# Kernel optimization log

Measured on AMD Instinct MI355X. Metric: run time of the kernel, lower is better.

The kernel has to match this reference:

```python
import jax, jax.numpy as jnp
import numpy as np

B, S, F, E, K = 4, 1024, 1024, 8, 2
H = 4 * F  # expert hidden dim, hard-coded as features*4 in the module


def setup_inputs() -> dict:
    key = jax.random.key(0)
    ks = jax.random.split(key, 7)
    def xavier(k, shape):
        fan_in, fan_out = shape[-2], shape[-1]
        scale = jnp.sqrt(6.0 / (fan_in + fan_out))
        return jax.random.uniform(k, shape, jnp.float32, -scale, scale)
    return {
        "x": jax.random.normal(ks[0], (B, S, F), jnp.float32),
        "Wg": xavier(ks[1], (F, E)),
        "bg": jnp.zeros((E,), jnp.float32),
        "W1": xavier(ks[2], (E, F, H)),
        "b1": jnp.zeros((E, H), jnp.float32),
        "W2": xavier(ks[3], (E, H, F)),
        "b2": jnp.zeros((E, F), jnp.float32),
    }


def reference(x, Wg, bg, W1, b1, W2, b2):
    # Gating: softmax over experts, keep top-k, renormalize.
    gate_probs = jax.nn.softmax(x @ Wg + bg, axis=-1)              # (b,s,E)
    k = K
    _, top_idx = jax.lax.top_k(gate_probs, k)                       # (b,s,k)
    expert_mask = jax.nn.one_hot(top_idx, gate_probs.shape[-1],
                                 dtype=gate_probs.dtype).sum(-2)    # (b,s,E)
    selected = gate_probs * expert_mask
    selected = selected / (selected.sum(-1, keepdims=True) + 1e-8)
    # Dense all-expert 2-layer MLP (gelu, tanh approximation as in flax nn.gelu).
    h = jax.nn.gelu(jnp.einsum('bsf,efh->bseh', x, W1) + b1)        # (b,s,E,H)
    expert_out = jnp.einsum('bseh,ehf->bsef', h, W2) + b2[None, None]  # (b,s,E,F)
    # Weighted combine over experts with renormalized top-k gates.
    return jnp.einsum('bsef,bse->bsf', expert_out, selected)
```

## Files before the change

kernel.cpp:

```cpp
#include <hip/hip_runtime.h>
#include <hip/hip_bf16.h>

constexpr int Ff = 1024;
constexpr int Ee = 8;
constexpr int Hh = 4096;
constexpr int T  = 4096;
constexpr int MB = 80;

typedef short     bf16x8 __attribute__((ext_vector_type(8)));
typedef float     f32x4  __attribute__((ext_vector_type(4)));
typedef unsigned short u16x8 __attribute__((ext_vector_type(8)));

__device__ __forceinline__ float gelu_fast(float v) {
  const float c2 = 2.0f * 0.7978845608028654f;
  float z2 = c2 * (v + 0.044715f * v * v * v);
  return v / (1.0f + __expf(-z2));
}

__device__ __forceinline__ unsigned short bf16bits(float f) {
  __hip_bfloat16 h = __float2bfloat16(f);
  return *reinterpret_cast<unsigned short*>(&h);
}

__device__ __forceinline__ void gl_lds16(const void* g, void* l) {
  __builtin_amdgcn_global_load_lds(
      (const __attribute__((address_space(1))) unsigned int*)g,
      (__attribute__((address_space(3))) unsigned int*)l, 16, 0, 0);
}

__global__ __launch_bounds__(256) void gating_kernel(
    const float* __restrict__ x, const float* __restrict__ Wg,
    const float* __restrict__ bg, int* __restrict__ cnt,
    int* __restrict__ list, float* __restrict__ wlist,
    int* __restrict__ done, int* __restrict__ offs) {
  const int wave = threadIdx.x >> 6;
  const int lane = threadIdx.x & 63;
  const int t = blockIdx.x * 4 + wave;
  float acc[Ee] = {0.f,0.f,0.f,0.f,0.f,0.f,0.f,0.f};
  const float* xrow = x + (size_t)t * Ff;
  for (int f0 = 0; f0 < Ff; f0 += 64) {
    float xv = xrow[f0 + lane];
    const float* wrow = Wg + (size_t)(f0 + lane) * Ee;
    float4 w0 = *reinterpret_cast<const float4*>(wrow);
    float4 w1 = *reinterpret_cast<const float4*>(wrow + 4);
    acc[0] += xv * w0.x; acc[1] += xv * w0.y;
    acc[2] += xv * w0.z; acc[3] += xv * w0.w;
    acc[4] += xv * w1.x; acc[5] += xv * w1.y;
    acc[6] += xv * w1.z; acc[7] += xv * w1.w;
  }
#pragma unroll
  for (int e = 0; e < Ee; ++e) {
#pragma unroll
    for (int off = 32; off; off >>= 1) acc[e] += __shfl_xor(acc[e], off);
  }
  if (lane == 0) {
    float l[Ee], m = -1e30f;
#pragma unroll
    for (int e = 0; e < Ee; ++e) { l[e] = acc[e] + bg[e]; m = fmaxf(m, l[e]); }
    float p[Ee], Z = 0.f;
#pragma unroll
    for (int e = 0; e < Ee; ++e) { p[e] = expf(l[e] - m); Z += p[e]; }
#pragma unroll
    for (int e = 0; e < Ee; ++e) p[e] /= Z;
    int i1 = 0; float p1 = p[0];
#pragma unroll
    for (int e = 1; e < Ee; ++e) if (p[e] > p1) { p1 = p[e]; i1 = e; }
    int i2 = -1; float p2 = -1e30f;
#pragma unroll
    for (int e = 0; e < Ee; ++e) if (e != i1 && p[e] > p2) { p2 = p[e]; i2 = e; }
    float denom = p1 + p2 + 1e-8f;
    int pos = atomicAdd(&cnt[i1], 1);
    list[i1 * T + pos] = t; wlist[i1 * T + pos] = p1 / denom;
    pos = atomicAdd(&cnt[i2], 1);
    list[i2 * T + pos] = t; wlist[i2 * T + pos] = p2 / denom;
  }
  __syncthreads();
  if (threadIdx.x == 0) {
    __threadfence();
    if (atomicAdd(done, 1) == gridDim.x - 1) {
      int s = 0;
#pragma unroll
      for (int e = 0; e < Ee; ++e) {
        offs[e] = s;
        s += (atomicAdd(&cnt[e], 0) + 127) & ~127;
      }
      offs[Ee] = s;
    }
  }
}

__global__ __launch_bounds__(256) void pack_w_kernel(
    const float* __restrict__ src1, unsigned short* __restrict__ dst1,
    int sN1, size_t s_estride1, size_t d_estride1, int KT1v, int NB1,
    const float* __restrict__ src2, unsigned short* __restrict__ dst2,
    int sN2, size_t s_estride2, size_t d_estride2, int KT2v, int NB2,
    int n1) {
  int idx = blockIdx.x;
  const float* src; unsigned short* dst;
  int sN, KT, nb, kt, e;
  size_t s_estride, d_estride;
  if (idx < n1) {
    src = src1; dst = dst1; sN = sN1; KT = KT1v;
    s_estride = s_estride1; d_estride = d_estride1;
    e = idx / (NB1 * KT1v); int r = idx % (NB1 * KT1v);
    nb = r / KT1v; kt = r % KT1v;
  } else {
    idx -= n1;
    src = src2; dst = dst2; sN = sN2; KT = KT2v;
    s_estride = s_estride2; d_estride = d_estride2;
    e = idx / (NB2 * KT2v); int r = idx % (NB2 * KT2v);
    nb = r / KT2v; kt = r % KT2v;
  }
  __shared__ float Ts[128][33];
  const int t = threadIdx.x;
  const float* sb = src + (size_t)e * s_estride + (size_t)(kt * 32) * sN + nb * 128;
  {
    const int row = t >> 5;
    const int cc  = (t & 31) * 4;
#pragma unroll
    for (int i = 0; i < 4; ++i) {
      float4 v = *reinterpret_cast<const float4*>(sb + (size_t)(row + 8 * i) * sN + cc);
      Ts[cc + 0][row + 8 * i] = v.x;
      Ts[cc + 1][row + 8 * i] = v.y;
      Ts[cc + 2][row + 8 * i] = v.z;
      Ts[cc + 3][row + 8 * i] = v.w;
    }
  }
  __syncthreads();
  unsigned short* db = dst + (size_t)e * d_estride + ((size_t)nb * KT + kt) * 4096;
#pragma unroll
  for (int j = 0; j < 2; ++j) {
    const int i2 = t + 256 * j;
    const int col = i2 & 127, kb = i2 >> 7;
    u16x8 o;
#pragma unroll
    for (int q = 0; q < 8; ++q) o[q] = bf16bits(Ts[col][kb * 8 + q]);
    *reinterpret_cast<u16x8*>(db + kb * 1024 + col * 8) = o;
  }
}

__global__ __launch_bounds__(256) void pack_x_kernel(
    const float* __restrict__ x, const int* __restrict__ cnt,
    const int* __restrict__ offs, const int* __restrict__ list,
    unsigned short* __restrict__ xg) {
  const int kt = blockIdx.x;
  const int mb = blockIdx.y;
  const int t = threadIdx.x;
  const int m0g = mb * 128;
  int e = 0;
#pragma unroll
  for (int i = 1; i < Ee; ++i) e += (m0g >= offs[i]) ? 1 : 0;
  const int ce = cnt[e];
  const int row = t >> 1, half = t & 1;
  const int mloc = m0g - offs[e] + row;
  const bool valid = (mloc >= 0) && (mloc < ce);
  const int token = valid ? list[e * T + mloc] : 0;
  const float* sp = x + (size_t)token * Ff + kt * 32 + half * 16;
  u16x8 o0, o1;
#pragma unroll
  for (int i = 0; i < 2; ++i) {
    float4 v = valid ? *reinterpret_cast<const float4*>(sp + i * 4)
                     : make_float4(0.f, 0.f, 0.f, 0.f);
    o0[i * 4 + 0] = bf16bits(v.x); o0[i * 4 + 1] = bf16bits(v.y);
    o0[i * 4 + 2] = bf16bits(v.z); o0[i * 4 + 3] = bf16bits(v.w);
  }
#pragma unroll
  for (int i = 2; i < 4; ++i) {
    float4 v = valid ? *reinterpret_cast<const float4*>(sp + i * 4)
                     : make_float4(0.f, 0.f, 0.f, 0.f);
    o1[(i - 2) * 4 + 0] = bf16bits(v.x); o1[(i - 2) * 4 + 1] = bf16bits(v.y);
    o1[(i - 2) * 4 + 2] = bf16bits(v.z); o1[(i - 2) * 4 + 3] = bf16bits(v.w);
  }
  unsigned short* db = xg + ((size_t)mb * (Ff / 32) + kt) * 4096 + row * 8;
  *reinterpret_cast<u16x8*>(db + (half * 2 + 0) * 1024) = o0;
  *reinterpret_cast<u16x8*>(db + (half * 2 + 1) * 1024) = o1;
}

__global__ __launch_bounds__(256, 3) void gemm1_mfma(
    const unsigned short* __restrict__ xg, const unsigned short* __restrict__ W1P,
    const float* __restrict__ b1, const int* __restrict__ cnt,
    const int* __restrict__ offs, unsigned short* __restrict__ hp, int Hc, int c) {
  const int nxg = Hc >> 7;
  const int nwg = nxg * MB;
  const int raw = blockIdx.x;
  int bid = (raw & 7) * (nwg >> 3) + (raw >> 3);
  const int bw = (nxg >= 4) ? 4 : nxg;
  const int band = bid / (MB * bw);
  const int r2 = bid % (MB * bw);
  const int by = r2 / bw;
  const int bx = band * bw + (r2 % bw);

  const int m0g = by * 128;
  int e = 0;
#pragma unroll
  for (int i = 1; i < Ee; ++i) e += (m0g >= offs[i]) ? 1 : 0;
  const int ce = cnt[e];
  const int mloc = m0g - offs[e];
  if (mloc >= ce) return;
  const int n0 = bx * 128;

  __shared__ __align__(16) unsigned short SMEM[24576];
  unsigned short* AsF = SMEM;
  unsigned short* BsF = SMEM + 12288;

  const int tid = threadIdx.x;
  const int w = tid >> 6, lane = tid & 63;
  const int g = lane >> 4, r16 = lane & 15;
  const int wr = w >> 1, wc = w & 1;

  constexpr int NT = Ff / 32;
  const unsigned short* aU = xg  + (size_t)by * NT * 4096;
  const unsigned short* bU = W1P + (size_t)(e * nxg + bx) * NT * 4096;

  f32x4 acc[4][4] = {};
  auto STAGE = [&](int buf, int kt) {
    const unsigned short* aS = aU + (size_t)kt * 4096 + w * 1024 + lane * 8;
    const unsigned short* bS = bU + (size_t)kt * 4096 + w * 1024 + lane * 8;
    unsigned short* aD = AsF + buf * 4096 + w * 1024;
    unsigned short* bD = BsF + buf * 4096 + w * 1024;
    gl_lds16(aS,       aD);
    gl_lds16(aS + 512, aD + 512);
    gl_lds16(bS,       bD);
    gl_lds16(bS + 512, bD + 512);
  };
  STAGE(0, 0); STAGE(1, 1); STAGE(2, 2);
  int cur = 0;
#pragma unroll 1
  for (int t = 0; t < NT; ++t) {
    const int rem = NT - t;
    if (rem >= 3)      asm volatile("s_waitcnt vmcnt(8)" ::: "memory");
    else if (rem == 2) asm volatile("s_waitcnt vmcnt(4)" ::: "memory");
    else               asm volatile("s_waitcnt vmcnt(0)" ::: "memory");
    __builtin_amdgcn_s_barrier();
    asm volatile("" ::: "memory");
    bf16x8 af[4], bfr[4];
#pragma unroll
    for (int i = 0; i < 4; ++i) {
      af[i]  = *reinterpret_cast<const bf16x8*>(
          AsF + cur * 4096 + g * 1024 + (wr * 64 + i * 16 + r16) * 8);
      bfr[i] = *reinterpret_cast<const bf16x8*>(
          BsF + cur * 4096 + g * 1024 + (wc * 64 + i * 16 + r16) * 8);
    }
    asm volatile("s_waitcnt lgkmcnt(0)" ::: "memory");
    __builtin_amdgcn_sched_barrier(0);
    __builtin_amdgcn_s_barrier();
    if (t + 3 < NT) STAGE(cur, t + 3);
    __builtin_amdgcn_s_setprio(1);
#pragma unroll
    for (int mi = 0; mi < 4; ++mi)
#pragma unroll
      for (int ni = 0; ni < 4; ++ni)
        acc[mi][ni] = __builtin_amdgcn_mfma_f32_16x16x32_bf16(
            af[mi], bfr[ni], acc[mi][ni], 0, 0, 0);
    __builtin_amdgcn_s_setprio(0);
    asm volatile("" ::: "memory");
    cur = (cur == 2) ? 0 : cur + 1;
  }
  __builtin_amdgcn_s_barrier();
  unsigned short (*Ls)[136] = reinterpret_cast<unsigned short(*)[136]>(SMEM);
#pragma unroll
  for (int ni = 0; ni < 4; ++ni) {
    const int col = wc * 64 + ni * 16 + r16;
    const float bias = b1[(size_t)e * Hh + (size_t)c * Hc + n0 + col];
#pragma unroll
    for (int mi = 0; mi < 4; ++mi)
#pragma unroll
      for (int r = 0; r < 4; ++r) {
        const int row = wr * 64 + mi * 16 + g * 4 + r;
        Ls[row][col] = bf16bits(gelu_fast(acc[mi][ni][r] + bias));
      }
  }
  __builtin_amdgcn_s_barrier();
  unsigned short* hb2 = hp + (size_t)by * (Hc >> 5) * 4096 + (size_t)(n0 >> 5) * 4096;
#pragma unroll
  for (int p = 0; p < 8; ++p) {
    const int u = p * 256 + tid;
    const int oct = u >> 7;
    const int row = u & 127;
    const int lc = oct * 8;
    unsigned short* dst = hb2 + ((size_t)((lc >> 5) * 4 + ((lc >> 3) & 3))) * 1024 + row * 8;
    *reinterpret_cast<u16x8*>(dst) = *reinterpret_cast<const u16x8*>(&Ls[row][lc]);
  }
}

__global__ __launch_bounds__(256, 3) void gemm2_mfma(
    const unsigned short* __restrict__ hp, const unsigned short* __restrict__ W2P,
    const float* __restrict__ b2, const int* __restrict__ cnt,
    const int* __restrict__ offs, const int* __restrict__ list,
    const float* __restrict__ wlist, float* __restrict__ out,
    int Hc, int biasC) {
  constexpr int nxg = Ff >> 7;
  const int nwg = nxg * MB;
  const int raw = blockIdx.x;
  int bid = (raw & 7) * (nwg >> 3) + (raw >> 3);
  const int bx = bid % nxg;
  const int by = bid / nxg;

  const int m0g = by * 128;
  int e = 0;
#pragma unroll
  for (int i = 1; i < Ee; ++i) e += (m0g >= offs[i]) ? 1 : 0;
  const int ce = cnt[e];
  const int mloc = m0g - offs[e];
  if (mloc >= ce) return;
  const int n0 = bx * 128;

  __shared__ __align__(16) unsigned short AsF[3 * 4096];
  __shared__ __align__(16) unsigned short BsF[3 * 4096];

  const int tid = threadIdx.x;
  const int w = tid >> 6, lane = tid & 63;
  const int g = lane >> 4, r16 = lane & 15;
  const int wr = w >> 1, wc = w & 1;

  const int KT2 = Hc >> 5;
  const int NT = KT2;
  const unsigned short* aU = hp  + (size_t)by * KT2 * 4096;
  const unsigned short* bU = W2P + (size_t)(e * nxg + bx) * KT2 * 4096;

  f32x4 acc[4][4] = {};
  auto STAGE = [&](int buf, int kt) {
    const unsigned short* aS = aU + (size_t)kt * 4096 + w * 1024 + lane * 8;
    const unsigned short* bS = bU + (size_t)kt * 4096 + w * 1024 + lane * 8;
    unsigned short* aD = AsF + buf * 4096 + w * 1024;
    unsigned short* bD = BsF + buf * 4096 + w * 1024;
    gl_lds16(aS,       aD);
    gl_lds16(aS + 512, aD + 512);
    gl_lds16(bS,       bD);
    gl_lds16(bS + 512, bD + 512);
  };
  STAGE(0, 0);
  if (NT > 1) STAGE(1, 1);
  if (NT > 2) STAGE(2, 2);
  int cur = 0;
#pragma unroll 1
  for (int t = 0; t < NT; ++t) {
    const int rem = NT - t;
    if (rem >= 3)      asm volatile("s_waitcnt vmcnt(8)" ::: "memory");
    else if (rem == 2) asm volatile("s_waitcnt vmcnt(4)" ::: "memory");
    else               asm volatile("s_waitcnt vmcnt(0)" ::: "memory");
    __builtin_amdgcn_s_barrier();
    asm volatile("" ::: "memory");
    bf16x8 af[4], bfr[4];
#pragma unroll
    for (int i = 0; i < 4; ++i) {
      af[i]  = *reinterpret_cast<const bf16x8*>(
          AsF + cur * 4096 + g * 1024 + (wr * 64 + i * 16 + r16) * 8);
      bfr[i] = *reinterpret_cast<const bf16x8*>(
          BsF + cur * 4096 + g * 1024 + (wc * 64 + i * 16 + r16) * 8);
    }
    asm volatile("s_waitcnt lgkmcnt(0)" ::: "memory");
    __builtin_amdgcn_sched_barrier(0);
    __builtin_amdgcn_s_barrier();
    if (t + 3 < NT) STAGE(cur, t + 3);
    __builtin_amdgcn_s_setprio(1);
#pragma unroll
    for (int mi = 0; mi < 4; ++mi)
#pragma unroll
      for (int ni = 0; ni < 4; ++ni)
        acc[mi][ni] = __builtin_amdgcn_mfma_f32_16x16x32_bf16(
            af[mi], bfr[ni], acc[mi][ni], 0, 0, 0);
    __builtin_amdgcn_s_setprio(0);
    asm volatile("" ::: "memory");
    cur = (cur == 2) ? 0 : cur + 1;
  }
  const bool addBias = (biasC != 0);
#pragma unroll
  for (int mi = 0; mi < 4; ++mi)
#pragma unroll
    for (int r = 0; r < 4; ++r) {
      const int row = wr * 64 + mi * 16 + g * 4 + r;
      if (mloc + row >= ce) continue;
      const int token = list[e * T + mloc + row];
      const float wgt = wlist[e * T + mloc + row];
      float* op = out + (size_t)token * Ff;
#pragma unroll
      for (int ni = 0; ni < 4; ++ni) {
        const int col = n0 + wc * 64 + ni * 16 + r16;
        float v = acc[mi][ni][r];
        if (addBias) v += b2[(size_t)e * Ff + col];
        atomicAdd(&op[col], wgt * v);
      }
    }
}

extern "C" void kernel_launch(void* const* d_in, const int* in_sizes, int n_in,
                              void* d_out, int out_size, void* d_ws, size_t ws_size,
                              hipStream_t stream) {
  const float* x  = (const float*)d_in[0];
  const float* Wg = (const float*)d_in[1];
  const float* bg = (const float*)d_in[2];
  const float* W1 = (const float*)d_in[3];
  const float* b1 = (const float*)d_in[4];
  const float* W2 = (const float*)d_in[5];
  const float* b2 = (const float*)d_in[6];
  float* out = (float*)d_out;

  const size_t fixed = 1024 + 2 * (size_t)T * Ee * 4 + (size_t)MB * 128 * Ff * 2;
  int Hc = 4096;
  while (Hc > 256 && fixed + (size_t)Hc * 53248 > ws_size) Hc >>= 1;
  const int nchunk = Hh / Hc;

  char* p = (char*)d_ws;
  int*   cnt   = (int*)p;            p += 256;
  int*   done  = (int*)p;            p += 256;
  int*   offs  = (int*)p;            p += 512;
  int*   list  = (int*)p;            p += (size_t)T * Ee * 4;
  float* wlist = (float*)p;          p += (size_t)T * Ee * 4;
  unsigned short* xg  = (unsigned short*)p;  p += (size_t)MB * 128 * Ff * 2;
  unsigned short* W1P = (unsigned short*)p;  p += (size_t)Ee * Hc * Ff * 2;
  unsigned short* W2P = (unsigned short*)p;  p += (size_t)Ee * Ff * Hc * 2;
  unsigned short* hp  = (unsigned short*)p;

  hipMemsetAsync(d_out, 0, (size_t)out_size * sizeof(float), stream);
  hipMemsetAsync(cnt, 0, 512, stream);

  gating_kernel<<<T / 4, 256, 0, stream>>>(x, Wg, bg, cnt, list, wlist, done, offs);
  pack_x_kernel<<<dim3(Ff / 32, MB), 256, 0, stream>>>(x, cnt, offs, list, xg);

  for (int c = 0; c < nchunk; ++c) {
    const int NB1 = Hc / 128, KT1v = Ff / 32;
    const int NB2 = Ff / 128, KT2v = Hc / 32;
    const int n1 = Ee * NB1 * KT1v;
    const int n2 = Ee * NB2 * KT2v;
    pack_w_kernel<<<n1 + n2, 256, 0, stream>>>(
        W1 + (size_t)c * Hc, W1P, Hh, (size_t)Ff * Hh, (size_t)Hc * Ff, KT1v, NB1,
        W2 + (size_t)c * Hc * Ff, W2P, Ff, (size_t)Hh * Ff, (size_t)Ff * Hc, KT2v, NB2,
        n1);
    gemm1_mfma<<<(Hc / 128) * MB, 256, 0, stream>>>(
        xg, W1P, b1, cnt, offs, hp, Hc, c);
    gemm2_mfma<<<(Ff / 128) * MB, 256, 0, stream>>>(
        hp, W2P, b2, cnt, offs, list, wlist, out, Hc,
        c == nchunk - 1 ? 1 : 0);
  }
}
```

Before: 435.1 us.

## Load A operand directly from global into registers, stage only B in LDS

Both grouped GEMM kernels now read the activation (A) tile fragments straight from global memory into registers, prefetched two k-steps ahead in a rotating set of four register buffers. Only the weight (B) tile still goes through the triple-buffered LDS pipeline. This cuts LDS traffic and shared-memory footprint, which could allow more occupancy, and removes the LDS read latency for A. In exchange it raises register pressure, issues uncoalesced-per-fragment global loads, and requires NT to be a multiple of 4 for the unrolled loop.

```diff
diff --git a/kernel.cpp b/kernel.cpp
--- a/kernel.cpp
+++ b/kernel.cpp
@@ -176,6 +176,64 @@
   *reinterpret_cast<u16x8*>(db + (half * 2 + 1) * 1024) = o1;
 }
 
+#define LOADA(PA, KT)                                                         \
+  _Pragma("unroll")                                                           \
+  for (int i_ = 0; i_ < 4; ++i_)                                              \
+    PA[i_] = *reinterpret_cast<const bf16x8*>(                                \
+        aU + (size_t)(KT) * 4096 + g * 1024 + (wr * 64 + i_ * 16 + r16) * 8);
+
+#define STAGEB(KT)                                                            \
+  {                                                                           \
+    const unsigned short* bS_ = bU + (size_t)(KT) * 4096 + w * 1024 + lane * 8; \
+    unsigned short* bD_ = BsF + ((KT) % 3) * 4096 + w * 1024;                 \
+    gl_lds16(bS_,       bD_);                                                 \
+    gl_lds16(bS_ + 512, bD_ + 512);                                           \
+  }
+
+#define GITER(T, PAU, PAL)                                                    \
+  {                                                                           \
+    const int t_ = (T);                                                       \
+    const int rem_ = NT - t_;                                                 \
+    if (t_ == 0 || rem_ == 1) asm volatile("s_waitcnt vmcnt(0)" ::: "memory");\
+    else if (rem_ >= 3)       asm volatile("s_waitcnt vmcnt(6)" ::: "memory");\
+    else                      asm volatile("s_waitcnt vmcnt(4)" ::: "memory");\
+    __builtin_amdgcn_s_barrier();                                             \
+    bf16x8 bfr_[4];                                                           \
+    const int cb_ = t_ % 3;                                                   \
+    _Pragma("unroll")                                                         \
+    for (int i_ = 0; i_ < 4; ++i_)                                            \
+      bfr_[i_] = *reinterpret_cast<const bf16x8*>(                            \
+          BsF + cb_ * 4096 + g * 1024 + (wc * 64 + i_ * 16 + r16) * 8);       \
+    asm volatile("s_waitcnt lgkmcnt(0)" ::: "memory");                        \
+    __builtin_amdgcn_sched_barrier(0);                                        \
+    __builtin_amdgcn_s_barrier();                                             \
+    if (t_ + 2 < NT) { LOADA(PAL, t_ + 2) }                                   \
+    if (t_ + 3 < NT) STAGEB(t_ + 3)                                           \
+    __builtin_amdgcn_s_setprio(1);                                            \
+    _Pragma("unroll")                                                         \
+    for (int mi_ = 0; mi_ < 4; ++mi_)                                         \
+      _Pragma("unroll")                                                       \
+      for (int ni_ = 0; ni_ < 4; ++ni_)                                       \
+        acc[mi_][ni_] = __builtin_amdgcn_mfma_f32_16x16x32_bf16(              \
+            PAU[mi_], bfr_[ni_], acc[mi_][ni_], 0, 0, 0);                     \
+    __builtin_amdgcn_s_setprio(0);                                            \
+    asm volatile("" ::: "memory");                                            \
+  }
+
+#define GEMM_CORE()                                                           \
+  f32x4 acc[4][4] = {};                                                       \
+  bf16x8 pa0[4], pa1[4], pa2[4], pa3[4];                                      \
+  LOADA(pa0, 0)                                                               \
+  LOADA(pa1, 1)                                                               \
+  STAGEB(0) STAGEB(1) STAGEB(2)                                               \
+  _Pragma("unroll 1")                                                         \
+  for (int t4 = 0; t4 < NT; t4 += 4) {                                        \
+    GITER(t4 + 0, pa0, pa2)                                                   \
+    GITER(t4 + 1, pa1, pa3)                                                   \
+    GITER(t4 + 2, pa2, pa0)                                                   \
+    GITER(t4 + 3, pa3, pa1)                                                   \
+  }
+
 __global__ __launch_bounds__(256, 3) void gemm1_mfma(
     const unsigned short* __restrict__ xg, const unsigned short* __restrict__ W1P,
     const float* __restrict__ b1, const int* __restrict__ cnt,
@@ -199,9 +257,8 @@
   if (mloc >= ce) return;
   const int n0 = bx * 128;
 
-  __shared__ __align__(16) unsigned short SMEM[24576];
-  unsigned short* AsF = SMEM;
-  unsigned short* BsF = SMEM + 12288;
+  __shared__ __align__(16) unsigned short SMEM[17408];
+  unsigned short* BsF = SMEM;
 
   const int tid = threadIdx.x;
   const int w = tid >> 6, lane = tid & 63;
@@ -212,50 +269,8 @@
   const unsigned short* aU = xg  + (size_t)by * NT * 4096;
   const unsigned short* bU = W1P + (size_t)(e * nxg + bx) * NT * 4096;
 
-  f32x4 acc[4][4] = {};
-  auto STAGE = [&](int buf, int kt) {
-    const unsigned short* aS = aU + (size_t)kt * 4096 + w * 1024 + lane * 8;
-    const unsigned short* bS = bU + (size_t)kt * 4096 + w * 1024 + lane * 8;
-    unsigned short* aD = AsF + buf * 4096 + w * 1024;
-    unsigned short* bD = BsF + buf * 4096 + w * 1024;
-    gl_lds16(aS,       aD);
-    gl_lds16(aS + 512, aD + 512);
-    gl_lds16(bS,       bD);
-    gl_lds16(bS + 512, bD + 512);
-  };
-  STAGE(0, 0); STAGE(1, 1); STAGE(2, 2);
-  int cur = 0;
-#pragma unroll 1
-  for (int t = 0; t < NT; ++t) {
-    const int rem = NT - t;
-    if (rem >= 3)      asm volatile("s_waitcnt vmcnt(8)" ::: "memory");
-    else if (rem == 2) asm volatile("s_waitcnt vmcnt(4)" ::: "memory");
-    else               asm volatile("s_waitcnt vmcnt(0)" ::: "memory");
-    __builtin_amdgcn_s_barrier();
-    asm volatile("" ::: "memory");
-    bf16x8 af[4], bfr[4];
-#pragma unroll
-    for (int i = 0; i < 4; ++i) {
-      af[i]  = *reinterpret_cast<const bf16x8*>(
-          AsF + cur * 4096 + g * 1024 + (wr * 64 + i * 16 + r16) * 8);
-      bfr[i] = *reinterpret_cast<const bf16x8*>(
-          BsF + cur * 4096 + g * 1024 + (wc * 64 + i * 16 + r16) * 8);
-    }
-    asm volatile("s_waitcnt lgkmcnt(0)" ::: "memory");
-    __builtin_amdgcn_sched_barrier(0);
-    __builtin_amdgcn_s_barrier();
-    if (t + 3 < NT) STAGE(cur, t + 3);
-    __builtin_amdgcn_s_setprio(1);
-#pragma unroll
-    for (int mi = 0; mi < 4; ++mi)
-#pragma unroll
-      for (int ni = 0; ni < 4; ++ni)
-        acc[mi][ni] = __builtin_amdgcn_mfma_f32_16x16x32_bf16(
-            af[mi], bfr[ni], acc[mi][ni], 0, 0, 0);
-    __builtin_amdgcn_s_setprio(0);
-    asm volatile("" ::: "memory");
-    cur = (cur == 2) ? 0 : cur + 1;
-  }
+  GEMM_CORE()
+
   __builtin_amdgcn_s_barrier();
   unsigned short (*Ls)[136] = reinterpret_cast<unsigned short(*)[136]>(SMEM);
 #pragma unroll
@@ -305,8 +320,8 @@
   if (mloc >= ce) return;
   const int n0 = bx * 128;
 
-  __shared__ __align__(16) unsigned short AsF[3 * 4096];
-  __shared__ __align__(16) unsigned short BsF[3 * 4096];
+  __shared__ __align__(16) unsigned short SMEM[12288];
+  unsigned short* BsF = SMEM;
 
   const int tid = threadIdx.x;
   const int w = tid >> 6, lane = tid & 63;
@@ -318,52 +333,8 @@
   const unsigned short* aU = hp  + (size_t)by * KT2 * 4096;
   const unsigned short* bU = W2P + (size_t)(e * nxg + bx) * KT2 * 4096;
 
-  f32x4 acc[4][4] = {};
-  auto STAGE = [&](int buf, int kt) {
-    const unsigned short* aS = aU + (size_t)kt * 4096 + w * 1024 + lane * 8;
-    const unsigned short* bS = bU + (size_t)kt * 4096 + w * 1024 + lane * 8;
-    unsigned short* aD = AsF + buf * 4096 + w * 1024;
-    unsigned short* bD = BsF + buf * 4096 + w * 1024;
-    gl_lds16(aS,       aD);
-    gl_lds16(aS + 512, aD + 512);
-    gl_lds16(bS,       bD);
-    gl_lds16(bS + 512, bD + 512);
-  };
-  STAGE(0, 0);
-  if (NT > 1) STAGE(1, 1);
-  if (NT > 2) STAGE(2, 2);
-  int cur = 0;
-#pragma unroll 1
-  for (int t = 0; t < NT; ++t) {
-    const int rem = NT - t;
-    if (rem >= 3)      asm volatile("s_waitcnt vmcnt(8)" ::: "memory");
-    else if (rem == 2) asm volatile("s_waitcnt vmcnt(4)" ::: "memory");
-    else               asm volatile("s_waitcnt vmcnt(0)" ::: "memory");
-    __builtin_amdgcn_s_barrier();
-    asm volatile("" ::: "memory");
-    bf16x8 af[4], bfr[4];
-#pragma unroll
-    for (int i = 0; i < 4; ++i) {
-      af[i]  = *reinterpret_cast<const bf16x8*>(
-          AsF + cur * 4096 + g * 1024 + (wr * 64 + i * 16 + r16) * 8);
-      bfr[i] = *reinterpret_cast<const bf16x8*>(
-          BsF + cur * 4096 + g * 1024 + (wc * 64 + i * 16 + r16) * 8);
-    }
-    asm volatile("s_waitcnt lgkmcnt(0)" ::: "memory");
-    __builtin_amdgcn_sched_barrier(0);
-    __builtin_amdgcn_s_barrier();
-    if (t + 3 < NT) STAGE(cur, t + 3);
-    __builtin_amdgcn_s_setprio(1);
-#pragma unroll
-    for (int mi = 0; mi < 4; ++mi)
-#pragma unroll
-      for (int ni = 0; ni < 4; ++ni)
-        acc[mi][ni] = __builtin_amdgcn_mfma_f32_16x16x32_bf16(
-            af[mi], bfr[ni], acc[mi][ni], 0, 0, 0);
-    __builtin_amdgcn_s_setprio(0);
-    asm volatile("" ::: "memory");
-    cur = (cur == 2) ? 0 : cur + 1;
-  }
+  GEMM_CORE()
+
   const bool addBias = (biasC != 0);
 #pragma unroll
   for (int mi = 0; mi < 4; ++mi)
```

Measured after the change: 526.7 us. 1.21x slower.
